# Kernel optimization log

Measured on AMD Instinct MI355X. Metric: run time of the kernel, lower is better.

## Reference

```python
import jax, jax.numpy as jnp
import numpy as np

N, F, A = 50000, 128, 128

def setup_inputs() -> dict:
    key = jax.random.key(0)
    ks = jax.random.split(key, 20)
    r = lambda i, shape: jax.random.normal(ks[i], shape, dtype=jnp.float32)
    w = lambda i, shape: jax.random.normal(ks[i], shape, dtype=jnp.float32) * 0.05
    return {
        "feat": r(0, (N, F)),
        "mu": r(1, (N, F, 3)),
        "T0": r(2, (N,)),
        "T1": r(3, (N, 3)),
        "T2": r(4, (N, 3, 3)),
        "T3": r(5, (N, 3, 3, 3)),
        # denseq: Dense(F,F,swish) -> Dense(F,F). Weights stored [in,out].
        "Wq1": w(6, (F, F)), "bq1": jnp.zeros((F,), jnp.float32),
        "Wq2": w(7, (F, F)), "bq2": jnp.zeros((F,), jnp.float32),
        "WT1": w(8, (F, F)),  # dense_T1, no bias
        "WT2": w(9, (F, F)),  # dense_T2, no bias
        "WT3": w(10, (F, F)), # dense_T3, no bias
        # dense_s: Dense(F,F,swish) -> Dense(F,A)
        "Ws1": w(11, (F, F)), "bs1": jnp.zeros((F,), jnp.float32),
        "Ws2": w(12, (F, A)), "bs2": jnp.zeros((A,), jnp.float32),
        "Wv": w(13, (F, A)),  # dense_v, no bias
    }

def reference(feat, mu, T0, T1, T2, T3,
              Wq1, bq1, Wq2, bq2, WT1, WT2, WT3,
              Ws1, bs1, Ws2, bs2, Wv):
    silu = jax.nn.silu  # swish
    # M0 = denseq(feat): [N, F]
    M0 = silu(feat @ Wq1 + bq1) @ Wq2 + bq2
    # M1/M2/M3: linear over feature dim of mu [N, F, 3]
    M1 = jnp.einsum('nfc,fg->ngc', mu, WT1)
    M2 = jnp.einsum('nfc,fg->ngc', mu, WT2)
    M3 = jnp.einsum('nfc,fg->ngc', mu, WT3)
    # scalar channel
    ms = jnp.sum(M1 * T1[:, None, :], axis=-1) + T0[:, None] * M0          # T1, T0 terms
    ms = ms + jnp.einsum('nfi,nfj,nij->nf', M2, M2, T2)                    # quadrupole . T2
    ms = ms + jnp.einsum('nfi,nfj,nfk,nijk->nf', M3, M3, M3, T3)           # octupole . T3
    # vector channel [N, F, 3]
    mv = T1[:, None, :] * M0[..., None]
    mv = mv + jnp.einsum('nij,nfj->nfi', T2, M1)
    mv = mv + jnp.einsum('nijk,nfj,nfk->nfi', T3, M2, M2)
    # output projections
    mv_out = jnp.einsum('nfc,fa->nac', mv, Wv)                             # [N, A, 3]
    ms_out = silu(ms @ Ws1 + bs1) @ Ws2 + bs2                              # [N, A]
    return ms_out, mv_out
```

## Files before the change

### kernel.cpp

```cpp
#include <hip/hip_runtime.h>
#include <cstdint>

#define N_NODES 50000
#define TILE 32
#define NBLK ((N_NODES + TILE - 1) / TILE)

typedef __bf16 bf16x8 __attribute__((ext_vector_type(8)));
typedef unsigned short ushort8_t __attribute__((ext_vector_type(8)));
typedef float f32x4 __attribute__((ext_vector_type(4)));

__device__ __forceinline__ unsigned short f2bf(float x) {
  union { float f; uint32_t u; } v; v.f = x;
  uint32_t r = v.u + 0x7FFFu + ((v.u >> 16) & 1u);
  return (unsigned short)(r >> 16);
}

__device__ __forceinline__ float fast_silu(float x) {
  return x / (1.0f + __expf(-x));
}

__global__ __launch_bounds__(256) void prep_weights(
    const float* __restrict__ Wq1, const float* __restrict__ Wq2,
    const float* __restrict__ WT1, const float* __restrict__ WT2,
    const float* __restrict__ WT3, const float* __restrict__ Ws1,
    const float* __restrict__ Ws2, const float* __restrict__ Wv,
    unsigned short* __restrict__ ws) {
  int tid = blockIdx.x * 256 + threadIdx.x;
  int w = tid >> 11;
  int rest = tid & 2047;
  int c = rest >> 8;
  int kt = (rest >> 6) & 3;
  int lane = rest & 63;
  int g = (lane & 15) + 16 * c;
  int k0 = kt * 32 + (lane >> 4) * 8;
  const float* srcs[8] = {Wq1, Wq2, WT1, WT2, WT3, Ws1, Ws2, Wv};
  const float* src = srcs[w];
  union { unsigned short u[8]; uint4 v; } o;
#pragma unroll
  for (int j = 0; j < 8; ++j) o.u[j] = f2bf(src[(k0 + j) * 128 + g]);
  *(uint4*)(ws + (size_t)w * 16384 + (size_t)rest * 8) = o.v;
}

__device__ __forceinline__ void gemm16(const unsigned short* sA,
                                       const unsigned short* sWp,
                                       int lane, int cb, f32x4 acc[2][2]) {
  const int m = lane & 15, q = lane >> 4;
  const f32x4 vzero = {0.f, 0.f, 0.f, 0.f};
#pragma unroll
  for (int rt = 0; rt < 2; ++rt)
#pragma unroll
    for (int cc = 0; cc < 2; ++cc) acc[rt][cc] = vzero;
#pragma unroll
  for (int kt = 0; kt < 4; ++kt) {
    const int k0 = q * 8 + kt * 32;
    bf16x8 a0 = __builtin_bit_cast(bf16x8, *(const ushort8_t*)(sA + m * 136 + k0));
    bf16x8 a1 = __builtin_bit_cast(bf16x8, *(const ushort8_t*)(sA + (m + 16) * 136 + k0));
#pragma unroll
    for (int cc = 0; cc < 2; ++cc) {
      bf16x8 b = __builtin_bit_cast(
          bf16x8, *(const ushort8_t*)(sWp + (((cb + cc) * 4 + kt) * 64 + lane) * 8));
      acc[0][cc] = __builtin_amdgcn_mfma_f32_16x16x32_bf16(a0, b, acc[0][cc], 0, 0, 0);
      acc[1][cc] = __builtin_amdgcn_mfma_f32_16x16x32_bf16(a1, b, acc[1][cc], 0, 0, 0);
    }
  }
}

__global__ __launch_bounds__(256, 2) void multipole_main(
    const float* __restrict__ feat, const float* __restrict__ mu,
    const float* __restrict__ T0g, const float* __restrict__ T1g,
    const float* __restrict__ T2g, const float* __restrict__ T3g,
    const float* __restrict__ bq1, const float* __restrict__ bq2,
    const float* __restrict__ bs1, const float* __restrict__ bs2,
    const unsigned short* __restrict__ ws, float* __restrict__ out) {
  __shared__ unsigned short sW[16384];
  __shared__ unsigned short sXmain[TILE * 136];
  __shared__ unsigned short sXmu[3][TILE * 136];
  __shared__ float sT[TILE][49];

  const int t = threadIdx.x;
  const int lane = t & 63, wv = t >> 6;
  const int m = lane & 15, q = lane >> 4;
  const int cb = wv * 2;
  const int nodeBase = blockIdx.x * TILE;

  auto stage_w = [&](int slot) {
    const uint4* src = (const uint4*)(ws + (size_t)slot * 16384);
    uint4* dst = (uint4*)sW;
#pragma unroll
    for (int i = 0; i < 8; ++i) dst[t + i * 256] = src[t + i * 256];
  };

  if (t < TILE) {
    int n = nodeBase + t;
    bool val = n < N_NODES;
    float t0 = val ? T0g[n] : 0.f;
    float t1[3], t2[9], t3[27];
#pragma unroll
    for (int i = 0; i < 3; ++i) t1[i] = val ? T1g[n * 3 + i] : 0.f;
#pragma unroll
    for (int i = 0; i < 9; ++i) t2[i] = val ? T2g[n * 9 + i] : 0.f;
#pragma unroll
    for (int i = 0; i < 27; ++i) t3[i] = val ? T3g[n * 27 + i] : 0.f;
    float* Tr = sT[t];
    Tr[0] = t0;
    Tr[1] = t1[0]; Tr[2] = t1[1]; Tr[3] = t1[2];
#pragma unroll
    for (int i = 0; i < 9; ++i) Tr[4 + i] = t2[i];
    Tr[13] = t2[0]; Tr[14] = t2[1] + t2[3]; Tr[15] = t2[2] + t2[6];
    Tr[16] = t2[4]; Tr[17] = t2[5] + t2[7]; Tr[18] = t2[8];
    Tr[19] = t3[0];
    Tr[20] = t3[1] + t3[3] + t3[9];
    Tr[21] = t3[2] + t3[6] + t3[18];
    Tr[22] = t3[4] + t3[10] + t3[12];
    Tr[23] = t3[5] + t3[7] + t3[11] + t3[15] + t3[19] + t3[21];
    Tr[24] = t3[8] + t3[20] + t3[24];
    Tr[25] = t3[13];
    Tr[26] = t3[14] + t3[16] + t3[22];
    Tr[27] = t3[17] + t3[23] + t3[25];
    Tr[28] = t3[26];
#pragma unroll
    for (int i = 0; i < 3; ++i) {
      const float* b = t3 + 9 * i;
      float* d = Tr + 29 + 6 * i;
      d[0] = b[0]; d[1] = b[1] + b[3]; d[2] = b[2] + b[6];
      d[3] = b[4]; d[4] = b[5] + b[7]; d[5] = b[8];
    }
  }

  {
    int node = t >> 3, f0 = (t & 7) * 16;
    int gn = nodeBase + node;
    union { unsigned short u[16]; uint4 v[2]; } buf;
    if (gn < N_NODES) {
      const float* p = feat + (size_t)gn * 128 + f0;
#pragma unroll
      for (int i = 0; i < 16; ++i) buf.u[i] = f2bf(p[i]);
    } else {
#pragma unroll
      for (int i = 0; i < 16; ++i) buf.u[i] = 0;
    }
    uint4* dst = (uint4*)&sXmain[node * 136 + f0];
    dst[0] = buf.v[0]; dst[1] = buf.v[1];
  }
  stage_w(0);
  __syncthreads();

  f32x4 A1[2][2], A2[2][2], A3[2][2];
  float msv[2][2][4];
  float mvv[3][2][2][4];

  gemm16(sXmain, sW, lane, cb, A1);
  float b0 = bq1[cb * 16 + m], b1 = bq1[cb * 16 + 16 + m];
  __syncthreads();
#pragma unroll
  for (int rt = 0; rt < 2; ++rt)
#pragma unroll
    for (int ri = 0; ri < 4; ++ri) {
      int lrow = rt * 16 + q * 4 + ri;
#pragma unroll
      for (int cc = 0; cc < 2; ++cc) {
        float h = fast_silu(A1[rt][cc][ri] + (cc ? b1 : b0));
        sXmain[lrow * 136 + (cb + cc) * 16 + m] = f2bf(h);
      }
    }
  stage_w(1);
  __syncthreads();

  gemm16(sXmain, sW, lane, cb, A1);
  {
    float bb0 = bq2[cb * 16 + m], bb1 = bq2[cb * 16 + 16 + m];
#pragma unroll
    for (int rt = 0; rt < 2; ++rt)
#pragma unroll
      for (int ri = 0; ri < 4; ++ri) {
        const float* Tr = sT[rt * 16 + q * 4 + ri];
        float t0 = Tr[0], ta = Tr[1], tb = Tr[2], tc = Tr[3];
#pragma unroll
        for (int cc = 0; cc < 2; ++cc) {
          float m0 = A1[rt][cc][ri] + (cc ? bb1 : bb0);
          msv[rt][cc][ri] = t0 * m0;
          mvv[0][rt][cc][ri] = ta * m0;
          mvv[1][rt][cc][ri] = tb * m0;
          mvv[2][rt][cc][ri] = tc * m0;
        }
      }
  }
  __syncthreads();

  {
    int node = t >> 3, f0 = (t & 7) * 16;
    int gn = nodeBase + node;
    union { unsigned short u[16]; uint4 v[2]; } b3[3];
    if (gn < N_NODES) {
      const float* p = mu + ((size_t)gn * 128 + f0) * 3;
#pragma unroll
      for (int i = 0; i < 16; ++i) {
        b3[0].u[i] = f2bf(p[i * 3 + 0]);
        b3[1].u[i] = f2bf(p[i * 3 + 1]);
        b3[2].u[i] = f2bf(p[i * 3 + 2]);
      }
    } else {
#pragma unroll
      for (int ch = 0; ch < 3; ++ch)
#pragma unroll
        for (int i = 0; i < 16; ++i) b3[ch].u[i] = 0;
    }
#pragma unroll
    for (int ch = 0; ch < 3; ++ch) {
      uint4* dst = (uint4*)&sXmu[ch][node * 136 + f0];
      dst[0] = b3[ch].v[0]; dst[1] = b3[ch].v[1];
    }
  }
  stage_w(2);
  __syncthreads();

#pragma unroll
  for (int ch = 0; ch < 3; ++ch) {
    gemm16(sXmu[ch], sW, lane, cb, A1);
#pragma unroll
    for (int rt = 0; rt < 2; ++rt)
#pragma unroll
      for (int ri = 0; ri < 4; ++ri) {
        const float* Tr = sT[rt * 16 + q * 4 + ri];
        float t1c = Tr[1 + ch];
        float u0 = Tr[4 + 0 + ch], u1 = Tr[4 + 3 + ch], u2 = Tr[4 + 6 + ch];
#pragma unroll
        for (int cc = 0; cc < 2; ++cc) {
          float v = A1[rt][cc][ri];
          msv[rt][cc][ri] += t1c * v;
          mvv[0][rt][cc][ri] += u0 * v;
          mvv[1][rt][cc][ri] += u1 * v;
          mvv[2][rt][cc][ri] += u2 * v;
        }
      }
  }
  __syncthreads();
  stage_w(4);
  __syncthreads();

  gemm16(sXmu[0], sW, lane, cb, A1);
  gemm16(sXmu[1], sW, lane, cb, A2);
  gemm16(sXmu[2], sW, lane, cb, A3);
#pragma unroll
  for (int rt = 0; rt < 2; ++rt)
#pragma unroll
    for (int ri = 0; ri < 4; ++ri) {
      const float* Cp = sT[rt * 16 + q * 4 + ri] + 19;
      float c0 = Cp[0], c1 = Cp[1], c2 = Cp[2], c3 = Cp[3], c4 = Cp[4];
      float c5 = Cp[5], c6 = Cp[6], c7 = Cp[7], c8 = Cp[8], c9 = Cp[9];
#pragma unroll
      for (int cc = 0; cc < 2; ++cc) {
        float u0 = A1[rt][cc][ri], u1 = A2[rt][cc][ri], u2 = A3[rt][cc][ri];
        float Q0 = u0 * u0, Q1 = u0 * u1, Q2 = u0 * u2;
        float Q3 = u1 * u1, Q4 = u1 * u2, Q5 = u2 * u2;
        msv[rt][cc][ri] += c0 * (Q0 * u0) + c1 * (Q0 * u1) + c2 * (Q0 * u2) +
                           c3 * (Q1 * u1) + c4 * (Q1 * u2) + c5 * (Q2 * u2) +
                           c6 * (Q3 * u1) + c7 * (Q3 * u2) + c8 * (Q4 * u2) +
                           c9 * (Q5 * u2);
      }
    }
  __syncthreads();
  stage_w(3);
  __syncthreads();

  gemm16(sXmu[0], sW, lane, cb, A1);
  gemm16(sXmu[1], sW, lane, cb, A2);
  gemm16(sXmu[2], sW, lane, cb, A3);
#pragma unroll
  for (int rt = 0; rt < 2; ++rt)
#pragma unroll
    for (int ri = 0; ri < 4; ++ri) {
      const float* Tr = sT[rt * 16 + q * 4 + ri];
      const float* q2 = Tr + 13;
      const float* d3 = Tr + 29;
      float q20 = q2[0], q21 = q2[1], q22 = q2[2], q23 = q2[3], q24 = q2[4], q25 = q2[5];
#pragma unroll
      for (int cc = 0; cc < 2; ++cc) {
        float v0 = A1[rt][cc][ri], v1 = A2[rt][cc][ri], v2 = A3[rt][cc][ri];
        float P0 = v0 * v0, P1 = v0 * v1, P2 = v0 * v2;
        float P3 = v1 * v1, P4 = v1 * v2, P5 = v2 * v2;
        msv[rt][cc][ri] += q20 * P0 + q21 * P1 + q22 * P2 + q23 * P3 + q24 * P4 + q25 * P5;
        mvv[0][rt][cc][ri] += d3[0] * P0 + d3[1] * P1 + d3[2] * P2 + d3[3] * P3 + d3[4] * P4 + d3[5] * P5;
        mvv[1][rt][cc][ri] += d3[6] * P0 + d3[7] * P1 + d3[8] * P2 + d3[9] * P3 + d3[10] * P4 + d3[11] * P5;
        mvv[2][rt][cc][ri] += d3[12] * P0 + d3[13] * P1 + d3[14] * P2 + d3[15] * P3 + d3[16] * P4 + d3[17] * P5;
      }
    }
  __syncthreads();

#pragma unroll
  for (int rt = 0; rt < 2; ++rt)
#pragma unroll
    for (int ri = 0; ri < 4; ++ri) {
      int lrow = rt * 16 + q * 4 + ri;
#pragma unroll
      for (int cc = 0; cc < 2; ++cc) {
        int col = (cb + cc) * 16 + m;
        sXmain[lrow * 136 + col] = f2bf(msv[rt][cc][ri]);
        sXmu[0][lrow * 136 + col] = f2bf(mvv[0][rt][cc][ri]);
        sXmu[1][lrow * 136 + col] = f2bf(mvv[1][rt][cc][ri]);
        sXmu[2][lrow * 136 + col] = f2bf(mvv[2][rt][cc][ri]);
      }
    }
  stage_w(5);
  __syncthreads();

  gemm16(sXmain, sW, lane, cb, A1);
  {
    float s0 = bs1[cb * 16 + m], s1 = bs1[cb * 16 + 16 + m];
    __syncthreads();
#pragma unroll
    for (int rt = 0; rt < 2; ++rt)
#pragma unroll
      for (int ri = 0; ri < 4; ++ri) {
        int lrow = rt * 16 + q * 4 + ri;
#pragma unroll
        for (int cc = 0; cc < 2; ++cc) {
          float g = fast_silu(A1[rt][cc][ri] + (cc ? s1 : s0));
          sXmain[lrow * 136 + (cb + cc) * 16 + m] = f2bf(g);
        }
      }
  }
  stage_w(6);
  __syncthreads();

  gemm16(sXmain, sW, lane, cb, A1);
  {
    float s0 = bs2[cb * 16 + m], s1 = bs2[cb * 16 + 16 + m];
#pragma unroll
    for (int rt = 0; rt < 2; ++rt)
#pragma unroll
      for (int ri = 0; ri < 4; ++ri) {
        int grow = nodeBase + rt * 16 + q * 4 + ri;
        if (grow < N_NODES) {
#pragma unroll
          for (int cc = 0; cc < 2; ++cc) {
            int col = (cb + cc) * 16 + m;
            out[(size_t)grow * 128 + col] = A1[rt][cc][ri] + (cc ? s1 : s0);
          }
        }
      }
  }
  __syncthreads();
  stage_w(7);
  __syncthreads();

  float* out2 = out + (size_t)N_NODES * 128;
#pragma unroll
  for (int ch = 0; ch < 3; ++ch) {
    gemm16(sXmu[ch], sW, lane, cb, A1);
#pragma unroll
    for (int rt = 0; rt < 2; ++rt)
#pragma unroll
      for (int ri = 0; ri < 4; ++ri) {
        int grow = nodeBase + rt * 16 + q * 4 + ri;
        if (grow < N_NODES) {
#pragma unroll
          for (int cc = 0; cc < 2; ++cc) {
            int col = (cb + cc) * 16 + m;
            out2[((size_t)grow * 128 + col) * 3 + ch] = A1[rt][cc][ri];
          }
        }
      }
  }
}

extern "C" void kernel_launch(void* const* d_in, const int* in_sizes, int n_in,
                              void* d_out, int out_size, void* d_ws, size_t ws_size,
                              hipStream_t stream) {
  const float* feat = (const float*)d_in[0];
  const float* mu   = (const float*)d_in[1];
  const float* T0   = (const float*)d_in[2];
  const float* T1   = (const float*)d_in[3];
  const float* T2   = (const float*)d_in[4];
  const float* T3   = (const float*)d_in[5];
  const float* Wq1  = (const float*)d_in[6];
  const float* bq1  = (const float*)d_in[7];
  const float* Wq2  = (const float*)d_in[8];
  const float* bq2  = (const float*)d_in[9];
  const float* WT1  = (const float*)d_in[10];
  const float* WT2  = (const float*)d_in[11];
  const float* WT3  = (const float*)d_in[12];
  const float* Ws1  = (const float*)d_in[13];
  const float* bs1  = (const float*)d_in[14];
  const float* Ws2  = (const float*)d_in[15];
  const float* bs2  = (const float*)d_in[16];
  const float* Wv   = (const float*)d_in[17];
  unsigned short* ws = (unsigned short*)d_ws;
  float* out = (float*)d_out;

  prep_weights<<<64, 256, 0, stream>>>(Wq1, Wq2, WT1, WT2, WT3, Ws1, Ws2, Wv, ws);
  multipole_main<<<NBLK, 256, 0, stream>>>(feat, mu, T0, T1, T2, T3,
                                           bq1, bq2, bs1, bs2, ws, out);
}
```

Baseline: 277.1 us.

## Read MFMA weight fragments directly from global memory instead of staging in LDS

Removes the shared-memory weight buffer and the per-stage copies and barriers that filled it. B fragments are now loaded straight from the prepacked global/L2 weights, and the three mu-channel GEMMs are merged so each B fragment is reused across the three channels. feat and mu are loaded up front, the Wv projection is moved before the dense_s MLP, and outputs use nontemporal stores. Occupancy is raised to 3 blocks per CU, traded against more global/L2 weight traffic per wave and higher register pressure.

```diff
diff --git a/kernel.cpp b/kernel.cpp
--- a/kernel.cpp
+++ b/kernel.cpp
@@ -4,6 +4,7 @@
 #define N_NODES 50000
 #define TILE 32
 #define NBLK ((N_NODES + TILE - 1) / TILE)
+#define SX 136
 
 typedef __bf16 bf16x8 __attribute__((ext_vector_type(8)));
 typedef unsigned short ushort8_t __attribute__((ext_vector_type(8)));
@@ -33,49 +34,94 @@
   int lane = rest & 63;
   int g = (lane & 15) + 16 * c;
   int k0 = kt * 32 + (lane >> 4) * 8;
-  const float* srcs[8] = {Wq1, Wq2, WT1, WT2, WT3, Ws1, Ws2, Wv};
-  const float* src = srcs[w];
+  const float* src = Wq1;
+  src = (w == 1) ? Wq2 : src;
+  src = (w == 2) ? WT1 : src;
+  src = (w == 3) ? WT2 : src;
+  src = (w == 4) ? WT3 : src;
+  src = (w == 5) ? Ws1 : src;
+  src = (w == 6) ? Ws2 : src;
+  src = (w == 7) ? Wv  : src;
   union { unsigned short u[8]; uint4 v; } o;
 #pragma unroll
   for (int j = 0; j < 8; ++j) o.u[j] = f2bf(src[(k0 + j) * 128 + g]);
   *(uint4*)(ws + (size_t)w * 16384 + (size_t)rest * 8) = o.v;
 }
 
-__device__ __forceinline__ void gemm16(const unsigned short* sA,
-                                       const unsigned short* sWp,
-                                       int lane, int cb, f32x4 acc[2][2]) {
+__device__ __forceinline__ bf16x8 bload(const unsigned short* __restrict__ wg,
+                                        int slot, int c, int kt, int lane) {
+  return __builtin_bit_cast(
+      bf16x8, *(const ushort8_t*)(wg + slot * 16384 + ((c * 4 + kt) * 64 + lane) * 8));
+}
+
+__device__ __forceinline__ bf16x8 aload(const unsigned short* sA, int row, int q, int kt) {
+  return __builtin_bit_cast(bf16x8, *(const ushort8_t*)(sA + row * SX + q * 8 + kt * 32));
+}
+
+__device__ __forceinline__ void gemm1(const unsigned short* sA,
+                                      const unsigned short* __restrict__ wg,
+                                      int slot, int lane, int cb, f32x4 acc[2][2]) {
   const int m = lane & 15, q = lane >> 4;
-  const f32x4 vzero = {0.f, 0.f, 0.f, 0.f};
-#pragma unroll
-  for (int rt = 0; rt < 2; ++rt)
-#pragma unroll
-    for (int cc = 0; cc < 2; ++cc) acc[rt][cc] = vzero;
+  const f32x4 vz = {0.f, 0.f, 0.f, 0.f};
+  acc[0][0] = vz; acc[0][1] = vz; acc[1][0] = vz; acc[1][1] = vz;
 #pragma unroll
   for (int kt = 0; kt < 4; ++kt) {
-    const int k0 = q * 8 + kt * 32;
-    bf16x8 a0 = __builtin_bit_cast(bf16x8, *(const ushort8_t*)(sA + m * 136 + k0));
-    bf16x8 a1 = __builtin_bit_cast(bf16x8, *(const ushort8_t*)(sA + (m + 16) * 136 + k0));
-#pragma unroll
-    for (int cc = 0; cc < 2; ++cc) {
-      bf16x8 b = __builtin_bit_cast(
-          bf16x8, *(const ushort8_t*)(sWp + (((cb + cc) * 4 + kt) * 64 + lane) * 8));
-      acc[0][cc] = __builtin_amdgcn_mfma_f32_16x16x32_bf16(a0, b, acc[0][cc], 0, 0, 0);
-      acc[1][cc] = __builtin_amdgcn_mfma_f32_16x16x32_bf16(a1, b, acc[1][cc], 0, 0, 0);
-    }
-  }
-}
-
-__global__ __launch_bounds__(256, 2) void multipole_main(
+    bf16x8 b0 = bload(wg, slot, cb, kt, lane);
+    bf16x8 b1 = bload(wg, slot, cb + 1, kt, lane);
+    bf16x8 a0 = aload(sA, m, q, kt);
+    bf16x8 a1 = aload(sA, m + 16, q, kt);
+    acc[0][0] = __builtin_amdgcn_mfma_f32_16x16x32_bf16(a0, b0, acc[0][0], 0, 0, 0);
+    acc[1][0] = __builtin_amdgcn_mfma_f32_16x16x32_bf16(a1, b0, acc[1][0], 0, 0, 0);
+    acc[0][1] = __builtin_amdgcn_mfma_f32_16x16x32_bf16(a0, b1, acc[0][1], 0, 0, 0);
+    acc[1][1] = __builtin_amdgcn_mfma_f32_16x16x32_bf16(a1, b1, acc[1][1], 0, 0, 0);
+  }
+}
+
+__device__ __forceinline__ void gemm3(const unsigned short* s0, const unsigned short* s1,
+                                      const unsigned short* s2,
+                                      const unsigned short* __restrict__ wg,
+                                      int slot, int lane, int cb,
+                                      f32x4 A1[2][2], f32x4 A2[2][2], f32x4 A3[2][2]) {
+  const int m = lane & 15, q = lane >> 4;
+  const f32x4 vz = {0.f, 0.f, 0.f, 0.f};
+  A1[0][0] = vz; A1[0][1] = vz; A1[1][0] = vz; A1[1][1] = vz;
+  A2[0][0] = vz; A2[0][1] = vz; A2[1][0] = vz; A2[1][1] = vz;
+  A3[0][0] = vz; A3[0][1] = vz; A3[1][0] = vz; A3[1][1] = vz;
+#pragma unroll
+  for (int kt = 0; kt < 4; ++kt) {
+    bf16x8 b0 = bload(wg, slot, cb, kt, lane);
+    bf16x8 b1 = bload(wg, slot, cb + 1, kt, lane);
+    bf16x8 a0 = aload(s0, m, q, kt);
+    bf16x8 a1 = aload(s0, m + 16, q, kt);
+    A1[0][0] = __builtin_amdgcn_mfma_f32_16x16x32_bf16(a0, b0, A1[0][0], 0, 0, 0);
+    A1[1][0] = __builtin_amdgcn_mfma_f32_16x16x32_bf16(a1, b0, A1[1][0], 0, 0, 0);
+    A1[0][1] = __builtin_amdgcn_mfma_f32_16x16x32_bf16(a0, b1, A1[0][1], 0, 0, 0);
+    A1[1][1] = __builtin_amdgcn_mfma_f32_16x16x32_bf16(a1, b1, A1[1][1], 0, 0, 0);
+    a0 = aload(s1, m, q, kt);
+    a1 = aload(s1, m + 16, q, kt);
+    A2[0][0] = __builtin_amdgcn_mfma_f32_16x16x32_bf16(a0, b0, A2[0][0], 0, 0, 0);
+    A2[1][0] = __builtin_amdgcn_mfma_f32_16x16x32_bf16(a1, b0, A2[1][0], 0, 0, 0);
+    A2[0][1] = __builtin_amdgcn_mfma_f32_16x16x32_bf16(a0, b1, A2[0][1], 0, 0, 0);
+    A2[1][1] = __builtin_amdgcn_mfma_f32_16x16x32_bf16(a1, b1, A2[1][1], 0, 0, 0);
+    a0 = aload(s2, m, q, kt);
+    a1 = aload(s2, m + 16, q, kt);
+    A3[0][0] = __builtin_amdgcn_mfma_f32_16x16x32_bf16(a0, b0, A3[0][0], 0, 0, 0);
+    A3[1][0] = __builtin_amdgcn_mfma_f32_16x16x32_bf16(a1, b0, A3[1][0], 0, 0, 0);
+    A3[0][1] = __builtin_amdgcn_mfma_f32_16x16x32_bf16(a0, b1, A3[0][1], 0, 0, 0);
+    A3[1][1] = __builtin_amdgcn_mfma_f32_16x16x32_bf16(a1, b1, A3[1][1], 0, 0, 0);
+  }
+}
+
+__global__ __launch_bounds__(256, 3) void multipole_main(
     const float* __restrict__ feat, const float* __restrict__ mu,
     const float* __restrict__ T0g, const float* __restrict__ T1g,
     const float* __restrict__ T2g, const float* __restrict__ T3g,
     const float* __restrict__ bq1, const float* __restrict__ bq2,
     const float* __restrict__ bs1, const float* __restrict__ bs2,
     const unsigned short* __restrict__ ws, float* __restrict__ out) {
-  __shared__ unsigned short sW[16384];
-  __shared__ unsigned short sXmain[TILE * 136];
-  __shared__ unsigned short sXmu[3][TILE * 136];
-  __shared__ float sT[TILE][49];
+  __shared__ unsigned short sXmain[TILE * SX];
+  __shared__ unsigned short sXmu[3][TILE * SX];
+  __shared__ float sT[TILE][47];
 
   const int t = threadIdx.x;
   const int lane = t & 63, wv = t >> 6;
@@ -83,13 +129,38 @@
   const int cb = wv * 2;
   const int nodeBase = blockIdx.x * TILE;
 
-  auto stage_w = [&](int slot) {
-    const uint4* src = (const uint4*)(ws + (size_t)slot * 16384);
-    uint4* dst = (uint4*)sW;
-#pragma unroll
-    for (int i = 0; i < 8; ++i) dst[t + i * 256] = src[t + i * 256];
-  };
-
+  {
+    int node = t >> 3, f0 = (t & 7) * 16;
+    int gn = nodeBase + node;
+    union { unsigned short u[16]; uint4 v[2]; } bf;
+    union { unsigned short u[16]; uint4 v[2]; } b3[3];
+    if (gn < N_NODES) {
+      const float* pf = feat + (size_t)gn * 128 + f0;
+      const float* pm = mu + ((size_t)gn * 128 + f0) * 3;
+#pragma unroll
+      for (int i = 0; i < 16; ++i) bf.u[i] = f2bf(pf[i]);
+#pragma unroll
+      for (int i = 0; i < 16; ++i) {
+        b3[0].u[i] = f2bf(pm[i * 3 + 0]);
+        b3[1].u[i] = f2bf(pm[i * 3 + 1]);
+        b3[2].u[i] = f2bf(pm[i * 3 + 2]);
+      }
+    } else {
+#pragma unroll
+      for (int i = 0; i < 16; ++i) bf.u[i] = 0;
+#pragma unroll
+      for (int ch = 0; ch < 3; ++ch)
+#pragma unroll
+        for (int i = 0; i < 16; ++i) b3[ch].u[i] = 0;
+    }
+    uint4* df = (uint4*)&sXmain[node * SX + f0];
+    df[0] = bf.v[0]; df[1] = bf.v[1];
+#pragma unroll
+    for (int ch = 0; ch < 3; ++ch) {
+      uint4* dm = (uint4*)&sXmu[ch][node * SX + f0];
+      dm[0] = b3[ch].v[0]; dm[1] = b3[ch].v[1];
+    }
+  }
   if (t < TILE) {
     int n = nodeBase + t;
     bool val = n < N_NODES;
@@ -126,30 +197,13 @@
       d[3] = b[4]; d[4] = b[5] + b[7]; d[5] = b[8];
     }
   }
-
-  {
-    int node = t >> 3, f0 = (t & 7) * 16;
-    int gn = nodeBase + node;
-    union { unsigned short u[16]; uint4 v[2]; } buf;
-    if (gn < N_NODES) {
-      const float* p = feat + (size_t)gn * 128 + f0;
-#pragma unroll
-      for (int i = 0; i < 16; ++i) buf.u[i] = f2bf(p[i]);
-    } else {
-#pragma unroll
-      for (int i = 0; i < 16; ++i) buf.u[i] = 0;
-    }
-    uint4* dst = (uint4*)&sXmain[node * 136 + f0];
-    dst[0] = buf.v[0]; dst[1] = buf.v[1];
-  }
-  stage_w(0);
   __syncthreads();
 
   f32x4 A1[2][2], A2[2][2], A3[2][2];
   float msv[2][2][4];
   float mvv[3][2][2][4];
 
-  gemm16(sXmain, sW, lane, cb, A1);
+  gemm1(sXmain, ws, 0, lane, cb, A1);
   float b0 = bq1[cb * 16 + m], b1 = bq1[cb * 16 + 16 + m];
   __syncthreads();
 #pragma unroll
@@ -158,15 +212,12 @@
     for (int ri = 0; ri < 4; ++ri) {
       int lrow = rt * 16 + q * 4 + ri;
 #pragma unroll
-      for (int cc = 0; cc < 2; ++cc) {
-        float h = fast_silu(A1[rt][cc][ri] + (cc ? b1 : b0));
-        sXmain[lrow * 136 + (cb + cc) * 16 + m] = f2bf(h);
-      }
-    }
-  stage_w(1);
-  __syncthreads();
-
-  gemm16(sXmain, sW, lane, cb, A1);
+      for (int cc = 0; cc < 2; ++cc)
+        sXmain[lrow * SX + (cb + cc) * 16 + m] = f2bf(fast_silu(A1[rt][cc][ri] + (cc ? b1 : b0)));
+    }
+  __syncthreads();
+
+  gemm1(sXmain, ws, 1, lane, cb, A1);
   {
     float bb0 = bq2[cb * 16 + m], bb1 = bq2[cb * 16 + 16 + m];
 #pragma unroll
@@ -185,62 +236,24 @@
         }
       }
   }
-  __syncthreads();
-
-  {
-    int node = t >> 3, f0 = (t & 7) * 16;
-    int gn = nodeBase + node;
-    union { unsigned short u[16]; uint4 v[2]; } b3[3];
-    if (gn < N_NODES) {
-      const float* p = mu + ((size_t)gn * 128 + f0) * 3;
-#pragma unroll
-      for (int i = 0; i < 16; ++i) {
-        b3[0].u[i] = f2bf(p[i * 3 + 0]);
-        b3[1].u[i] = f2bf(p[i * 3 + 1]);
-        b3[2].u[i] = f2bf(p[i * 3 + 2]);
-      }
-    } else {
-#pragma unroll
-      for (int ch = 0; ch < 3; ++ch)
-#pragma unroll
-        for (int i = 0; i < 16; ++i) b3[ch].u[i] = 0;
-    }
-#pragma unroll
-    for (int ch = 0; ch < 3; ++ch) {
-      uint4* dst = (uint4*)&sXmu[ch][node * 136 + f0];
-      dst[0] = b3[ch].v[0]; dst[1] = b3[ch].v[1];
-    }
-  }
-  stage_w(2);
-  __syncthreads();
-
-#pragma unroll
-  for (int ch = 0; ch < 3; ++ch) {
-    gemm16(sXmu[ch], sW, lane, cb, A1);
-#pragma unroll
-    for (int rt = 0; rt < 2; ++rt)
-#pragma unroll
-      for (int ri = 0; ri < 4; ++ri) {
-        const float* Tr = sT[rt * 16 + q * 4 + ri];
-        float t1c = Tr[1 + ch];
-        float u0 = Tr[4 + 0 + ch], u1 = Tr[4 + 3 + ch], u2 = Tr[4 + 6 + ch];
-#pragma unroll
-        for (int cc = 0; cc < 2; ++cc) {
-          float v = A1[rt][cc][ri];
-          msv[rt][cc][ri] += t1c * v;
-          mvv[0][rt][cc][ri] += u0 * v;
-          mvv[1][rt][cc][ri] += u1 * v;
-          mvv[2][rt][cc][ri] += u2 * v;
-        }
-      }
-  }
-  __syncthreads();
-  stage_w(4);
-  __syncthreads();
-
-  gemm16(sXmu[0], sW, lane, cb, A1);
-  gemm16(sXmu[1], sW, lane, cb, A2);
-  gemm16(sXmu[2], sW, lane, cb, A3);
+
+  gemm3(sXmu[0], sXmu[1], sXmu[2], ws, 2, lane, cb, A1, A2, A3);
+#pragma unroll
+  for (int rt = 0; rt < 2; ++rt)
+#pragma unroll
+    for (int ri = 0; ri < 4; ++ri) {
+      const float* Tr = sT[rt * 16 + q * 4 + ri];
+#pragma unroll
+      for (int cc = 0; cc < 2; ++cc) {
+        float v0 = A1[rt][cc][ri], v1 = A2[rt][cc][ri], v2 = A3[rt][cc][ri];
+        msv[rt][cc][ri] += Tr[1] * v0 + Tr[2] * v1 + Tr[3] * v2;
+        mvv[0][rt][cc][ri] += Tr[4] * v0 + Tr[5] * v1 + Tr[6] * v2;
+        mvv[1][rt][cc][ri] += Tr[7] * v0 + Tr[8] * v1 + Tr[9] * v2;
+        mvv[2][rt][cc][ri] += Tr[10] * v0 + Tr[11] * v1 + Tr[12] * v2;
+      }
+    }
+
+  gemm3(sXmu[0], sXmu[1], sXmu[2], ws, 4, lane, cb, A1, A2, A3);
 #pragma unroll
   for (int rt = 0; rt < 2; ++rt)
 #pragma unroll
@@ -259,13 +272,8 @@
                            c9 * (Q5 * u2);
       }
     }
-  __syncthreads();
-  stage_w(3);
-  __syncthreads();
-
-  gemm16(sXmu[0], sW, lane, cb, A1);
-  gemm16(sXmu[1], sW, lane, cb, A2);
-  gemm16(sXmu[2], sW, lane, cb, A3);
+
+  gemm3(sXmu[0], sXmu[1], sXmu[2], ws, 3, lane, cb, A1, A2, A3);
 #pragma unroll
   for (int rt = 0; rt < 2; ++rt)
 #pragma unroll
@@ -295,16 +303,33 @@
 #pragma unroll
       for (int cc = 0; cc < 2; ++cc) {
         int col = (cb + cc) * 16 + m;
-        sXmain[lrow * 136 + col] = f2bf(msv[rt][cc][ri]);
-        sXmu[0][lrow * 136 + col] = f2bf(mvv[0][rt][cc][ri]);
-        sXmu[1][lrow * 136 + col] = f2bf(mvv[1][rt][cc][ri]);
-        sXmu[2][lrow * 136 + col] = f2bf(mvv[2][rt][cc][ri]);
-      }
-    }
-  stage_w(5);
-  __syncthreads();
-
-  gemm16(sXmain, sW, lane, cb, A1);
+        sXmain[lrow * SX + col] = f2bf(msv[rt][cc][ri]);
+        sXmu[0][lrow * SX + col] = f2bf(mvv[0][rt][cc][ri]);
+        sXmu[1][lrow * SX + col] = f2bf(mvv[1][rt][cc][ri]);
+        sXmu[2][lrow * SX + col] = f2bf(mvv[2][rt][cc][ri]);
+      }
+    }
+  __syncthreads();
+
+  gemm1(sXmain, ws, 5, lane, cb, A1);
+  float* out2 = out + (size_t)N_NODES * 128;
+#pragma unroll
+  for (int ch = 0; ch < 3; ++ch) {
+    gemm1(sXmu[ch], ws, 7, lane, cb, A2);
+#pragma unroll
+    for (int rt = 0; rt < 2; ++rt)
+#pragma unroll
+      for (int ri = 0; ri < 4; ++ri) {
+        int grow = nodeBase + rt * 16 + q * 4 + ri;
+        if (grow < N_NODES) {
+#pragma unroll
+          for (int cc = 0; cc < 2; ++cc) {
+            int col = (cb + cc) * 16 + m;
+            __builtin_nontemporal_store(A2[rt][cc][ri], &out2[((size_t)grow * 128 + col) * 3 + ch]);
+          }
+        }
+      }
+  }
   {
     float s0 = bs1[cb * 16 + m], s1 = bs1[cb * 16 + 16 + m];
     __syncthreads();
@@ -314,16 +339,13 @@
       for (int ri = 0; ri < 4; ++ri) {
         int lrow = rt * 16 + q * 4 + ri;
 #pragma unroll
-        for (int cc = 0; cc < 2; ++cc) {
-          float g = fast_silu(A1[rt][cc][ri] + (cc ? s1 : s0));
-          sXmain[lrow * 136 + (cb + cc) * 16 + m] = f2bf(g);
-        }
-      }
-  }
-  stage_w(6);
-  __syncthreads();
-
-  gemm16(sXmain, sW, lane, cb, A1);
+        for (int cc = 0; cc < 2; ++cc)
+          sXmain[lrow * SX + (cb + cc) * 16 + m] = f2bf(fast_silu(A1[rt][cc][ri] + (cc ? s1 : s0)));
+      }
+  }
+  __syncthreads();
+
+  gemm1(sXmain, ws, 6, lane, cb, A1);
   {
     float s0 = bs2[cb * 16 + m], s1 = bs2[cb * 16 + 16 + m];
 #pragma unroll
@@ -335,29 +357,7 @@
 #pragma unroll
           for (int cc = 0; cc < 2; ++cc) {
             int col = (cb + cc) * 16 + m;
-            out[(size_t)grow * 128 + col] = A1[rt][cc][ri] + (cc ? s1 : s0);
-          }
-        }
-      }
-  }
-  __syncthreads();
-  stage_w(7);
-  __syncthreads();
-
-  float* out2 = out + (size_t)N_NODES * 128;
-#pragma unroll
-  for (int ch = 0; ch < 3; ++ch) {
-    gemm16(sXmu[ch], sW, lane, cb, A1);
-#pragma unroll
-    for (int rt = 0; rt < 2; ++rt)
-#pragma unroll
-      for (int ri = 0; ri < 4; ++ri) {
-        int grow = nodeBase + rt * 16 + q * 4 + ri;
-        if (grow < N_NODES) {
-#pragma unroll
-          for (int cc = 0; cc < 2; ++cc) {
-            int col = (cb + cc) * 16 + m;
-            out2[((size_t)grow * 128 + col) * 3 + ch] = A1[rt][cc][ri];
+            __builtin_nontemporal_store(A1[rt][cc][ri] + (cc ? s1 : s0), &out[(size_t)grow * 128 + col]);
           }
         }
       }
```

After: 432.2 us. 56.0% more time.
